# Kernel optimization log

Measured on AMD Instinct MI355X. Metric: run time of the kernel, lower is better.

## Reference

```python
import jax, jax.numpy as jnp
import numpy as np

KERNEL_MUL = 2.0
KERNEL_NUM = 5


def setup_inputs() -> dict:
    key = jax.random.key(0)
    k1, k2 = jax.random.split(key)
    source_features = jax.random.normal(k1, (4096, 1024), dtype=jnp.float32)
    target_features = jax.random.normal(k2, (4096, 1024), dtype=jnp.float32)
    return {"source_features": source_features, "target_features": target_features}


def reference(source_features, target_features):
    n = source_features.shape[0]
    total = jnp.concatenate([source_features, target_features], axis=0)  # [L, D]
    L = total.shape[0]
    # Pairwise squared distances via gram trick (same math as sum((a-b)**2)).
    sq = jnp.sum(total * total, axis=1)  # [L]
    d2 = jnp.maximum(sq[:, None] + sq[None, :] - 2.0 * (total @ total.T), 0.0)  # [L, L]
    # Median-heuristic-style bandwidth: mean of off-diagonal distances.
    bandwidth = jnp.sum(d2) / (L * L - L)
    bandwidth = bandwidth / (KERNEL_MUL ** (KERNEL_NUM // 2))
    # Multi-bandwidth RBF kernel sum (fixed small loop over KERNEL_NUM).
    kernel = jnp.zeros_like(d2)
    for i in range(KERNEL_NUM):
        kernel = kernel + jnp.exp(-d2 / (bandwidth * (KERNEL_MUL ** i)))
    kernel = kernel / KERNEL_NUM
    ss = jnp.mean(kernel[:n, :n])
    tt = jnp.mean(kernel[n:, n:])
    st = jnp.mean(kernel[:n, n:])
    return ss + tt - 2.0 * st
```

## Files before the change

### kernel.cpp

```cpp
#include <hip/hip_runtime.h>
#include <hip/hip_bf16.h>
#include <stdint.h>


#define L_TOTAL 8192
#define D_FEAT  1024
#define N_HALF  4096
#define TILE    128
#define TTILES  64
#define NBLK    (TTILES*(TTILES+1)/2)
#define BK      64

typedef __bf16 bf16_t;
typedef __bf16 bf16x4_t __attribute__((ext_vector_type(4)));
typedef __bf16 bf16x8_t __attribute__((ext_vector_type(8)));
typedef float  f32x4_t  __attribute__((ext_vector_type(4)));

#define XB_OFF   0
#define SQ_OFF   (L_TOTAL * D_FEAT * 2)
#define COL_OFF  (SQ_OFF + L_TOTAL * 4)
#define SACC_OFF (COL_OFF + D_FEAT * 4)
#define C1_OFF   (SACC_OFF + 8)

__device__ __forceinline__ void async_ld16(void* lds, const void* g) {
  auto ldsp = (__attribute__((address_space(3))) void*)(uintptr_t)lds;
  auto gp   = (const __attribute__((address_space(1))) void*)(uintptr_t)g;
  __builtin_amdgcn_global_load_lds(gp, ldsp, 16, 0, 0);
}

extern "C" __global__ __launch_bounds__(256) void k_zero(
    float* __restrict__ colsum, double* __restrict__ S_acc)
{
  const int tid = threadIdx.x;
  for (int c = tid; c < D_FEAT; c += 256) colsum[c] = 0.f;
  if (tid == 0) *S_acc = 0.0;
}

extern "C" __global__ __launch_bounds__(256) void k_prep(
    const float* __restrict__ src, const float* __restrict__ tgt,
    bf16_t* __restrict__ Xb, float* __restrict__ sq, float* __restrict__ colsum)
{
  __shared__ float cs[4][D_FEAT];
  const int tid  = threadIdx.x;
  const int lane = tid & 63;
  const int w    = tid >> 6;
  const int rbase = blockIdx.x * 32 + w * 8;

  float csp[16];
  #pragma unroll
  for (int j = 0; j < 16; ++j) csp[j] = 0.f;

  for (int i = 0; i < 8; ++i) {
    const int row = rbase + i;
    const float* xr = (row < N_HALF) ? (src + (size_t)row * D_FEAT)
                                     : (tgt + (size_t)(row - N_HALF) * D_FEAT);
    float s = 0.f;
    #pragma unroll
    for (int q = 0; q < 4; ++q) {
      const float4 v = ((const float4*)xr)[q * 64 + lane];
      bf16x4_t bv;
      bv[0] = (bf16_t)v.x; bv[1] = (bf16_t)v.y; bv[2] = (bf16_t)v.z; bv[3] = (bf16_t)v.w;
      *(bf16x4_t*)(Xb + (size_t)row * D_FEAT + (q * 64 + lane) * 4) = bv;
      const float g0 = (float)bv[0], g1 = (float)bv[1], g2 = (float)bv[2], g3 = (float)bv[3];
      s += g0 * g0 + g1 * g1 + g2 * g2 + g3 * g3;
      csp[q * 4 + 0] += v.x; csp[q * 4 + 1] += v.y;
      csp[q * 4 + 2] += v.z; csp[q * 4 + 3] += v.w;
    }
    #pragma unroll
    for (int off = 32; off > 0; off >>= 1) s += __shfl_down(s, off);
    if (lane == 0) sq[row] = s;
  }

  #pragma unroll
  for (int q = 0; q < 4; ++q) {
    float4 v4 = make_float4(csp[q*4+0], csp[q*4+1], csp[q*4+2], csp[q*4+3]);
    *(float4*)&cs[w][(q * 64 + lane) * 4] = v4;
  }
  __syncthreads();
  #pragma unroll
  for (int k = 0; k < 4; ++k) {
    const int c = tid * 4 + k;
    atomicAdd(&colsum[c], cs[0][c] + cs[1][c] + cs[2][c] + cs[3][c]);
  }
}

extern "C" __global__ __launch_bounds__(1024) void k_bw(
    const float* __restrict__ sq, const float* __restrict__ colsum,
    float* __restrict__ c1out)
{
  const int tid = threadIdx.x;
  double t = 0.0;
  for (int i = tid; i < L_TOTAL; i += 1024) t += (double)sq[i];
  t *= 2.0 * (double)L_TOTAL;
  if (tid < D_FEAT) { double v = colsum[tid]; t -= 2.0 * v * v; }
  __shared__ double red[1024];
  red[tid] = t;
  __syncthreads();
  for (int off = 512; off > 0; off >>= 1) {
    if (tid < off) red[tid] += red[tid + off];
    __syncthreads();
  }
  if (tid == 0) {
    double bw = red[0] / ((double)L_TOTAL * (double)L_TOTAL - (double)L_TOTAL);
    bw = bw / 4.0;
    *c1out = (float)(-1.4426950408889634 / (16.0 * bw));
  }
}

extern "C" __global__ __launch_bounds__(256) void k_mmd(
    const bf16_t* __restrict__ Xb, const float* __restrict__ sq,
    const float* __restrict__ c1ptr, double* __restrict__ S_acc)
{
  __shared__ __align__(16) char smem[2 * TILE * BK * 2];
  bf16_t* As = (bf16_t*)smem;
  bf16_t* Bs = (bf16_t*)(smem + TILE * BK * 2);

  const int b = (blockIdx.x & 7) * (NBLK / 8) + (blockIdx.x >> 3);
  int ti = (int)((sqrtf(8.f * (float)b + 1.f) - 1.f) * 0.5f);
  while ((ti + 1) * (ti + 2) / 2 <= b) ++ti;
  while (ti * (ti + 1) / 2 > b) --ti;
  const int tj = b - ti * (ti + 1) / 2;
  const int row0 = ti * TILE, col0 = tj * TILE;

  const int tid  = threadIdx.x;
  const int lane = tid & 63;
  const int w    = tid >> 6;
  const int wr   = w >> 1, wc = w & 1;

  const int srow = lane >> 3;
  const int scol = ((lane & 7) ^ srow) * 8;
  uint32_t offA[4], offB[4];
  #pragma unroll
  for (int q = 0; q < 4; ++q) {
    const int ch = w * 4 + q;
    offA[q] = (uint32_t)(row0 + ch * 8 + srow) * D_FEAT + scol;
    offB[q] = (uint32_t)(col0 + ch * 8 + srow) * D_FEAT + scol;
  }

  const int x = lane >> 4, y = lane & 7, rlo = lane & 15;
  const int baA0 = (wr * 64 + rlo) * (BK * 2) + ((x ^ y) * 16);
  const int baB0 = (wc * 64 + rlo) * (BK * 2) + ((x ^ y) * 16);
  const int baA1 = baA0 ^ 64;
  const int baB1 = baB0 ^ 64;
  const char* Ac = (const char*)As;
  const char* Bc = (const char*)Bs;

  f32x4_t acc[4][4] = {};

  for (int k0 = 0; k0 < D_FEAT; k0 += BK) {
    #pragma unroll
    for (int q = 0; q < 4; ++q) {
      async_ld16(&As[(w * 4 + q) * 512], Xb + offA[q] + k0);
      async_ld16(&Bs[(w * 4 + q) * 512], Xb + offB[q] + k0);
    }
    __syncthreads();

    bf16x8_t af0[4], af1[4], bf0[4], bf1[4];
    #pragma unroll
    for (int m = 0; m < 4; ++m) {
      af0[m] = *(const bf16x8_t*)(Ac + baA0 + m * 2048);
      af1[m] = *(const bf16x8_t*)(Ac + baA1 + m * 2048);
    }
    #pragma unroll
    for (int n = 0; n < 4; ++n) {
      bf0[n] = *(const bf16x8_t*)(Bc + baB0 + n * 2048);
      bf1[n] = *(const bf16x8_t*)(Bc + baB1 + n * 2048);
    }
    #pragma unroll
    for (int m = 0; m < 4; ++m)
      #pragma unroll
      for (int n = 0; n < 4; ++n)
        acc[m][n] = __builtin_amdgcn_mfma_f32_16x16x32_bf16(af0[m], bf0[n], acc[m][n], 0, 0, 0);
    #pragma unroll
    for (int m = 0; m < 4; ++m)
      #pragma unroll
      for (int n = 0; n < 4; ++n)
        acc[m][n] = __builtin_amdgcn_mfma_f32_16x16x32_bf16(af1[m], bf1[n], acc[m][n], 0, 0, 0);
    __syncthreads();
  }

  const float c1   = *c1ptr;
  const float sgn  = ((ti < TTILES / 2) == (tj < TTILES / 2)) ? 1.f : -1.f;
  const float wgt  = (ti == tj ? 1.f : 2.f) * sgn;
  float part = 0.f;
  const int colb = col0 + wc * 64 + rlo;
  const int rowb = row0 + wr * 64 + x * 4;
  #pragma unroll
  for (int m = 0; m < 4; ++m) {
    #pragma unroll
    for (int n = 0; n < 4; ++n) {
      const float sqj = sq[colb + n * 16];
      #pragma unroll
      for (int r = 0; r < 4; ++r) {
        const float sqi = sq[rowb + m * 16 + r];
        float d2 = fmaxf(sqi + sqj - 2.f * acc[m][n][r], 0.f);
        const float e  = __builtin_amdgcn_exp2f(d2 * c1);
        const float e2 = e * e, e4 = e2 * e2, e8 = e4 * e4, e16 = e8 * e8;
        part += e + e2 + e4 + e8 + e16;
      }
    }
  }
  part *= wgt;

  #pragma unroll
  for (int off = 32; off > 0; off >>= 1) part += __shfl_down(part, off);
  float* red = (float*)smem;
  __syncthreads();
  if (lane == 0) red[w] = part;
  __syncthreads();
  if (tid == 0)
    atomicAdd(S_acc, (double)(red[0] + red[1] + red[2] + red[3]));
}

extern "C" __global__ void k_fin(const double* __restrict__ S_acc, float* __restrict__ out)
{
  out[0] = (float)(*S_acc / (5.0 * (double)N_HALF * (double)N_HALF));
}

extern "C" void kernel_launch(void* const* d_in, const int* in_sizes, int n_in,
                              void* d_out, int out_size, void* d_ws, size_t ws_size,
                              hipStream_t stream) {
  const float* src = (const float*)d_in[0];
  const float* tgt = (const float*)d_in[1];
  float* out = (float*)d_out;
  char* ws = (char*)d_ws;
  bf16_t* Xb     = (bf16_t*)(ws + XB_OFF);
  float*  sq     = (float*)(ws + SQ_OFF);
  float*  colsum = (float*)(ws + COL_OFF);
  double* S_acc  = (double*)(ws + SACC_OFF);
  float*  c1     = (float*)(ws + C1_OFF);

  k_zero<<<1, 256, 0, stream>>>(colsum, S_acc);
  k_prep<<<256, 256, 0, stream>>>(src, tgt, Xb, sq, colsum);
  k_bw  <<<1, 1024, 0, stream>>>(sq, colsum, c1);
  k_mmd <<<NBLK, 256, 0, stream>>>(Xb, sq, c1, S_acc);
  k_fin <<<1, 1, 0, stream>>>(S_acc, out);
}
```

Before: 221.6 us.

## Double-buffer GEMM tiles and fold bandwidth/finalize kernels into main kernel

```diff
diff --git a/kernel.cpp b/kernel.cpp
--- a/kernel.cpp
+++ b/kernel.cpp
@@ -10,6 +10,7 @@
 #define TTILES  64
 #define NBLK    (TTILES*(TTILES+1)/2)
 #define BK      64
+#define NT      (D_FEAT / BK)
 
 typedef __bf16 bf16_t;
 typedef __bf16 bf16x4_t __attribute__((ext_vector_type(4)));
@@ -18,22 +19,17 @@
 
 #define XB_OFF   0
 #define SQ_OFF   (L_TOTAL * D_FEAT * 2)
-#define COL_OFF  (SQ_OFF + L_TOTAL * 4)
-#define SACC_OFF (COL_OFF + D_FEAT * 4)
-#define C1_OFF   (SACC_OFF + 8)
+#define MS_OFF   (SQ_OFF + L_TOTAL * 4)
+#define SACC_OFF (MS_OFF)
+#define C1_OFF   (MS_OFF + 8)
+#define CTR_OFF  (MS_OFF + 12)
+#define COL_OFF  (MS_OFF + 16)
+#define MS_BYTES (16 + D_FEAT * 4)
 
 __device__ __forceinline__ void async_ld16(void* lds, const void* g) {
   auto ldsp = (__attribute__((address_space(3))) void*)(uintptr_t)lds;
   auto gp   = (const __attribute__((address_space(1))) void*)(uintptr_t)g;
   __builtin_amdgcn_global_load_lds(gp, ldsp, 16, 0, 0);
-}
-
-extern "C" __global__ __launch_bounds__(256) void k_zero(
-    float* __restrict__ colsum, double* __restrict__ S_acc)
-{
-  const int tid = threadIdx.x;
-  for (int c = tid; c < D_FEAT; c += 256) colsum[c] = 0.f;
-  if (tid == 0) *S_acc = 0.0;
 }
 
 extern "C" __global__ __launch_bounds__(256) void k_prep(
@@ -44,13 +40,14 @@
   const int tid  = threadIdx.x;
   const int lane = tid & 63;
   const int w    = tid >> 6;
-  const int rbase = blockIdx.x * 32 + w * 8;
+  const int rbase = blockIdx.x * 16 + w * 4;
 
   float csp[16];
   #pragma unroll
   for (int j = 0; j < 16; ++j) csp[j] = 0.f;
 
-  for (int i = 0; i < 8; ++i) {
+  #pragma unroll
+  for (int i = 0; i < 4; ++i) {
     const int row = rbase + i;
     const float* xr = (row < N_HALF) ? (src + (size_t)row * D_FEAT)
                                      : (tgt + (size_t)(row - N_HALF) * D_FEAT);
@@ -84,36 +81,45 @@
   }
 }
 
-extern "C" __global__ __launch_bounds__(1024) void k_bw(
-    const float* __restrict__ sq, const float* __restrict__ colsum,
-    float* __restrict__ c1out)
-{
-  const int tid = threadIdx.x;
-  double t = 0.0;
-  for (int i = tid; i < L_TOTAL; i += 1024) t += (double)sq[i];
-  t *= 2.0 * (double)L_TOTAL;
-  if (tid < D_FEAT) { double v = colsum[tid]; t -= 2.0 * v * v; }
-  __shared__ double red[1024];
-  red[tid] = t;
-  __syncthreads();
-  for (int off = 512; off > 0; off >>= 1) {
-    if (tid < off) red[tid] += red[tid + off];
-    __syncthreads();
-  }
-  if (tid == 0) {
-    double bw = red[0] / ((double)L_TOTAL * (double)L_TOTAL - (double)L_TOTAL);
-    bw = bw / 4.0;
-    *c1out = (float)(-1.4426950408889634 / (16.0 * bw));
-  }
-}
-
 extern "C" __global__ __launch_bounds__(256) void k_mmd(
     const bf16_t* __restrict__ Xb, const float* __restrict__ sq,
-    const float* __restrict__ c1ptr, double* __restrict__ S_acc)
+    const float* __restrict__ colsum, float* __restrict__ c1w,
+    double* __restrict__ S_acc, unsigned* __restrict__ ctr,
+    float* __restrict__ out)
 {
-  __shared__ __align__(16) char smem[2 * TILE * BK * 2];
-  bf16_t* As = (bf16_t*)smem;
-  bf16_t* Bs = (bf16_t*)(smem + TILE * BK * 2);
+  __shared__ __align__(16) bf16_t Abuf[2][TILE * BK];
+  __shared__ __align__(16) bf16_t Bbuf[2][TILE * BK];
+
+  const int tid  = threadIdx.x;
+  const int lane = tid & 63;
+  const int w    = tid >> 6;
+  const int wr   = w >> 1, wc = w & 1;
+
+  float c1_local = 0.f;
+  if (blockIdx.x == 0) {
+    double t = 0.0;
+    for (int i = tid; i < L_TOTAL; i += 256) t += (double)sq[i];
+    t *= 2.0 * (double)L_TOTAL;
+    double u = 0.0;
+    #pragma unroll
+    for (int k = 0; k < 4; ++k) { double v = colsum[tid * 4 + k]; u += v * v; }
+    t -= 2.0 * u;
+    double* red2 = (double*)Abuf;
+    red2[tid] = t;
+    __syncthreads();
+    for (int off = 128; off > 0; off >>= 1) {
+      if (tid < off) red2[tid] += red2[tid + off];
+      __syncthreads();
+    }
+    double bw = red2[0] / ((double)L_TOTAL * (double)L_TOTAL - (double)L_TOTAL);
+    bw = bw / 4.0;
+    c1_local = (float)(-1.4426950408889634 / (16.0 * bw));
+    if (tid == 0) {
+      __hip_atomic_store((unsigned*)c1w, __builtin_bit_cast(unsigned, c1_local),
+                         __ATOMIC_RELEASE, __HIP_MEMORY_SCOPE_AGENT);
+    }
+  }
+  __syncthreads();
 
   const int b = (blockIdx.x & 7) * (NBLK / 8) + (blockIdx.x >> 3);
   int ti = (int)((sqrtf(8.f * (float)b + 1.f) - 1.f) * 0.5f);
@@ -122,11 +128,6 @@
   const int tj = b - ti * (ti + 1) / 2;
   const int row0 = ti * TILE, col0 = tj * TILE;
 
-  const int tid  = threadIdx.x;
-  const int lane = tid & 63;
-  const int w    = tid >> 6;
-  const int wr   = w >> 1, wc = w & 1;
-
   const int srow = lane >> 3;
   const int scol = ((lane & 7) ^ srow) * 8;
   uint32_t offA[4], offB[4];
@@ -140,31 +141,30 @@
   const int x = lane >> 4, y = lane & 7, rlo = lane & 15;
   const int baA0 = (wr * 64 + rlo) * (BK * 2) + ((x ^ y) * 16);
   const int baB0 = (wc * 64 + rlo) * (BK * 2) + ((x ^ y) * 16);
-  const int baA1 = baA0 ^ 64;
-  const int baB1 = baB0 ^ 64;
-  const char* Ac = (const char*)As;
-  const char* Bc = (const char*)Bs;
 
   f32x4_t acc[4][4] = {};
 
-  for (int k0 = 0; k0 < D_FEAT; k0 += BK) {
+  auto stage = [&](bf16_t* Ad, bf16_t* Bd, int kt) {
+    const int kofs = kt * BK;
     #pragma unroll
     for (int q = 0; q < 4; ++q) {
-      async_ld16(&As[(w * 4 + q) * 512], Xb + offA[q] + k0);
-      async_ld16(&Bs[(w * 4 + q) * 512], Xb + offB[q] + k0);
-    }
-    __syncthreads();
-
+      async_ld16(&Ad[(w * 4 + q) * 512], Xb + offA[q] + kofs);
+      async_ld16(&Bd[(w * 4 + q) * 512], Xb + offB[q] + kofs);
+    }
+  };
+  auto compute = [&](const bf16_t* As, const bf16_t* Bs) {
+    const char* Ac = (const char*)As;
+    const char* Bc = (const char*)Bs;
     bf16x8_t af0[4], af1[4], bf0[4], bf1[4];
     #pragma unroll
     for (int m = 0; m < 4; ++m) {
-      af0[m] = *(const bf16x8_t*)(Ac + baA0 + m * 2048);
-      af1[m] = *(const bf16x8_t*)(Ac + baA1 + m * 2048);
+      af0[m] = *(const bf16x8_t*)(Ac + (baA0 + m * 2048));
+      af1[m] = *(const bf16x8_t*)(Ac + ((baA0 + m * 2048) ^ 64));
     }
     #pragma unroll
     for (int n = 0; n < 4; ++n) {
-      bf0[n] = *(const bf16x8_t*)(Bc + baB0 + n * 2048);
-      bf1[n] = *(const bf16x8_t*)(Bc + baB1 + n * 2048);
+      bf0[n] = *(const bf16x8_t*)(Bc + (baB0 + n * 2048));
+      bf1[n] = *(const bf16x8_t*)(Bc + ((baB0 + n * 2048) ^ 64));
     }
     #pragma unroll
     for (int m = 0; m < 4; ++m)
@@ -176,10 +176,29 @@
       #pragma unroll
       for (int n = 0; n < 4; ++n)
         acc[m][n] = __builtin_amdgcn_mfma_f32_16x16x32_bf16(af1[m], bf1[n], acc[m][n], 0, 0, 0);
+  };
+
+  stage(Abuf[0], Bbuf[0], 0);
+  __syncthreads();
+  #pragma unroll 2
+  for (int t = 0; t < NT; ++t) {
+    const int cur = t & 1, nxt = cur ^ 1;
+    if (t + 1 < NT) stage(Abuf[nxt], Bbuf[nxt], t + 1);
+    compute(Abuf[cur], Bbuf[cur]);
     __syncthreads();
   }
 
-  const float c1   = *c1ptr;
+  float c1;
+  if (blockIdx.x == 0) {
+    c1 = c1_local;
+  } else {
+    unsigned v;
+    while ((v = __hip_atomic_load((const unsigned*)c1w, __ATOMIC_ACQUIRE,
+                                  __HIP_MEMORY_SCOPE_AGENT)) == 0u)
+      __builtin_amdgcn_s_sleep(8);
+    c1 = __builtin_bit_cast(float, v);
+  }
+
   const float sgn  = ((ti < TTILES / 2) == (tj < TTILES / 2)) ? 1.f : -1.f;
   const float wgt  = (ti == tj ? 1.f : 2.f) * sgn;
   float part = 0.f;
@@ -204,17 +223,20 @@
 
   #pragma unroll
   for (int off = 32; off > 0; off >>= 1) part += __shfl_down(part, off);
-  float* red = (float*)smem;
+  float* red = (float*)Abuf;
   __syncthreads();
   if (lane == 0) red[w] = part;
   __syncthreads();
-  if (tid == 0)
+  if (tid == 0) {
     atomicAdd(S_acc, (double)(red[0] + red[1] + red[2] + red[3]));
-}
-
-extern "C" __global__ void k_fin(const double* __restrict__ S_acc, float* __restrict__ out)
-{
-  out[0] = (float)(*S_acc / (5.0 * (double)N_HALF * (double)N_HALF));
+    __threadfence();
+    const unsigned old = atomicAdd(ctr, 1u);
+    if (old == NBLK - 1) {
+      __threadfence();
+      const double S = atomicAdd(S_acc, 0.0);
+      out[0] = (float)(S / (5.0 * (double)N_HALF * (double)N_HALF));
+    }
+  }
 }
 
 extern "C" void kernel_launch(void* const* d_in, const int* in_sizes, int n_in,
@@ -224,15 +246,14 @@
   const float* tgt = (const float*)d_in[1];
   float* out = (float*)d_out;
   char* ws = (char*)d_ws;
-  bf16_t* Xb     = (bf16_t*)(ws + XB_OFF);
-  float*  sq     = (float*)(ws + SQ_OFF);
-  float*  colsum = (float*)(ws + COL_OFF);
-  double* S_acc  = (double*)(ws + SACC_OFF);
-  float*  c1     = (float*)(ws + C1_OFF);
-
-  k_zero<<<1, 256, 0, stream>>>(colsum, S_acc);
-  k_prep<<<256, 256, 0, stream>>>(src, tgt, Xb, sq, colsum);
-  k_bw  <<<1, 1024, 0, stream>>>(sq, colsum, c1);
-  k_mmd <<<NBLK, 256, 0, stream>>>(Xb, sq, c1, S_acc);
-  k_fin <<<1, 1, 0, stream>>>(S_acc, out);
-}
+  bf16_t*   Xb     = (bf16_t*)(ws + XB_OFF);
+  float*    sq     = (float*)(ws + SQ_OFF);
+  double*   S_acc  = (double*)(ws + SACC_OFF);
+  float*    c1w    = (float*)(ws + C1_OFF);
+  unsigned* ctr    = (unsigned*)(ws + CTR_OFF);
+  float*    colsum = (float*)(ws + COL_OFF);
+
+  hipMemsetAsync(ws + MS_OFF, 0, MS_BYTES, stream);
+  k_prep<<<512, 256, 0, stream>>>(src, tgt, Xb, sq, colsum);
+  k_mmd <<<NBLK, 256, 0, stream>>>(Xb, sq, colsum, c1w, S_acc, ctr, out);
+}
```

Result: slower. 373.5 us (+68.5%).
